# Performance work log

Hardware: AMD Instinct MI355X
Metric: run time of the kernel (lower is better)

The kernel has to match this reference:

```python
import jax, jax.numpy as jnp
import numpy as np

N, N_FEAT, F1, F2, F3, N_Z = 4096, 512, 256, 128, 64, 16
SLOPE = 0.2
NEG = -9e16


def _xavier(key, shape):
    std = (2.0 / (shape[0] + shape[1])) ** 0.5
    return jax.random.normal(key, shape, dtype=jnp.float32) * std


def setup_inputs() -> dict:
    key = jax.random.key(0)
    ks = jax.random.split(key, 20)
    x = jax.random.normal(ks[0], (N, N_FEAT), dtype=jnp.float32)
    adj = jax.random.randint(ks[1], (N, N), 0, 2, dtype=jnp.int32)
    dims = [N_FEAT, F1, F2, F3, N_Z, F3, F2, F1, N_FEAT]
    inp = {"x": x, "adj": adj}
    for i in range(8):
        fi, fo = dims[i], dims[i + 1]
        inp[f"w{i+1}"] = _xavier(ks[2 + 2 * i], (fi, fo))
        inp[f"a{i+1}"] = _xavier(ks[3 + 2 * i], (2 * fo, 1))
    return inp


def _gat(x, adj_pos, w, a):
    h = x @ w                               # [N, f_out]
    f = h.shape[1]
    src = h @ a[:f]                         # [N, 1]
    tgt = h @ a[f:]                         # [N, 1]
    e = jax.nn.leaky_relu(src + tgt.T, SLOPE)  # [N, N] broadcast score sum
    e = jnp.where(adj_pos, e, NEG)
    attn = jax.nn.softmax(e, axis=-1)
    return attn @ h                          # [N, f_out]


def reference(x, adj, w1, a1, w2, a2, w3, a3, w4, a4, w5, a5, w6, a6, w7, a7, w8, a8):
    adj_pos = adj > 0
    h1 = _gat(x, adj_pos, w1, a1)
    h2 = _gat(h1, adj_pos, w2, a2)
    h3 = _gat(h2, adj_pos, w3, a3)
    h4 = _gat(h3, adj_pos, w4, a4)
    h5 = _gat(h4, adj_pos, w5, a5)
    h6 = _gat(h5, adj_pos, w6, a6)
    h7 = _gat(h6, adj_pos, w7, a7)
    x_bar = _gat(h7, adj_pos, w8, a8)
    return (x_bar, h1, h2, h3, h4)
```

## Files before the change

### kernel.cpp

```cpp
#include <hip/hip_runtime.h>
#include <hip/hip_bf16.h>
#include <hip/hip_fp16.h>


#define NROWS 4096
#define TMC 12.0f

typedef __attribute__((ext_vector_type(8))) short v8s;
typedef __attribute__((ext_vector_type(8))) _Float16 v8h;
typedef __attribute__((ext_vector_type(2))) _Float16 h2v;
typedef __attribute__((ext_vector_type(4))) float v4f;

__device__ inline unsigned short f2bf(float x) {
  union { float f; unsigned u; } v; v.f = x;
  unsigned r = v.u + 0x7fffu + ((v.u >> 16) & 1u);
  return (unsigned short)(r >> 16);
}

__global__ void pack_adj(const int* __restrict__ adj, unsigned long long* __restrict__ bits) {
  int row = blockIdx.x;
  int lane = threadIdx.x & 63, wave = threadIdx.x >> 6;
  for (int w = wave; w < 64; w += 4) {
    unsigned long long m = __ballot(adj[(size_t)row * NROWS + w * 64 + lane] > 0);
    if (lane == 0) bits[row * 64 + w] = m;
  }
}

struct WTArgs { const float* src[8]; unsigned short* dst[8]; int K[8]; int F[8]; };
__global__ void transpose_w(WTArgs A) {
  int z = blockIdx.z;
  const float* in = A.src[z];
  unsigned short* out = A.dst[z];
  int R = A.K[z], C = A.F[z];
  __shared__ unsigned short tile[32][33];
  int c0 = blockIdx.x * 32, r0 = blockIdx.y * 32;
  if (c0 >= C || r0 >= R) return;
#pragma unroll
  for (int dy = 0; dy < 32; dy += 8) {
    int r = r0 + threadIdx.y + dy, c = c0 + threadIdx.x;
    if (r < R && c < C) tile[threadIdx.y + dy][threadIdx.x] = f2bf(in[(size_t)r * C + c]);
  }
  __syncthreads();
#pragma unroll
  for (int dy = 0; dy < 32; dy += 8) {
    int c = c0 + threadIdx.y + dy, r = r0 + threadIdx.x;
    if (r < R && c < C) out[(size_t)c * R + r] = tile[threadIdx.x][threadIdx.y + dy];
  }
}

__global__ __launch_bounds__(128) void gemm_xw(const float* __restrict__ A,
                                               const unsigned short* __restrict__ BT,
                                               float* __restrict__ C,
                                               unsigned short* __restrict__ HTt,
                                               int K, int Nf) {
  __shared__ unsigned short zone[64 * 36];
  int lane = threadIdx.x & 63, wave = threadIdx.x >> 6;
  int quad = lane >> 4, l16 = lane & 15;
  int row0 = blockIdx.x * 32 + wave * 16;
  int col0 = blockIdx.y * 64;
  int nf = Nf - col0; nf = nf > 64 ? 4 : (nf + 15) / 16;
  v4f acc[4] = {{0.f,0.f,0.f,0.f},{0.f,0.f,0.f,0.f},{0.f,0.f,0.f,0.f},{0.f,0.f,0.f,0.f}};
  for (int k0 = 0; k0 < K; k0 += 32) {
    int kk = k0 + quad * 8;
    v8s a = {0,0,0,0,0,0,0,0};
    if (kk < K) {
      float4 f0 = *(const float4*)(A + (size_t)(row0 + l16) * K + kk);
      float4 f1 = *(const float4*)(A + (size_t)(row0 + l16) * K + kk + 4);
      union { v8s s; __hip_bfloat162 h[4]; } ua;
      ua.h[0] = __float22bfloat162_rn(make_float2(f0.x, f0.y));
      ua.h[1] = __float22bfloat162_rn(make_float2(f0.z, f0.w));
      ua.h[2] = __float22bfloat162_rn(make_float2(f1.x, f1.y));
      ua.h[3] = __float22bfloat162_rn(make_float2(f1.z, f1.w));
      a = ua.s;
    }
    for (int t = 0; t < nf; t++) {
      v8s b = {0,0,0,0,0,0,0,0};
      if (kk < K) b = *(const v8s*)(BT + (size_t)(col0 + t * 16 + l16) * K + kk);
      acc[t] = __builtin_amdgcn_mfma_f32_16x16x32_bf16(a, b, acc[t], 0, 0, 0);
    }
  }
  for (int t = 0; t < nf; t++) {
#pragma unroll
    for (int r = 0; r < 4; r++) {
      float v = acc[t][r];
      C[(size_t)(row0 + quad * 4 + r) * Nf + col0 + t * 16 + l16] = v;
      union { _Float16 h; unsigned short s; } cv; cv.h = (_Float16)v;
      zone[(t * 16 + l16) * 36 + wave * 16 + quad * 4 + r] = cv.s;
    }
  }
  __syncthreads();
  unsigned* dst = (unsigned*)(HTt + (size_t)(blockIdx.x) * Nf * 32 + (size_t)col0 * 32);
  const unsigned* zsrc = (const unsigned*)zone;
  int total = nf * 256;
  for (int idx = threadIdx.x; idx < total; idx += 128) {
    int f = idx >> 4, jp = idx & 15;
    dst[idx] = zsrc[f * 18 + jp];
  }
}

__global__ void gemv_srctgt(const float* __restrict__ H, const float* __restrict__ a,
                            float* __restrict__ src, unsigned short* __restrict__ Ev16,
                            unsigned short* __restrict__ Gv16, int f) {
  int row = blockIdx.x * 4 + (threadIdx.x >> 6);
  int lane = threadIdx.x & 63;
  float s = 0.f, t = 0.f;
  for (int k = lane; k < f; k += 64) {
    float h = H[(size_t)row * f + k];
    s += h * a[k];
    t += h * a[f + k];
  }
#pragma unroll
  for (int off = 32; off; off >>= 1) { s += __shfl_down(s, off); t += __shfl_down(t, off); }
  if (lane == 0) {
    src[row] = s;
    union { _Float16 h; unsigned short u; } ce, cg;
    ce.h = (_Float16)(__expf(t - TMC) * 16384.f);
    cg.h = (_Float16)(__expf(0.2f * (t - TMC)) * 16.f);
    Ev16[row] = ce.u;
    Gv16[row] = cg.u;
  }
}

template<int NF>
__global__ __launch_bounds__(256) void pass2f(const unsigned* __restrict__ adjW,
                                              const float* __restrict__ src,
                                              const unsigned short* __restrict__ Ev16,
                                              const unsigned short* __restrict__ Gv16,
                                              const unsigned short* __restrict__ HTt,
                                              float* __restrict__ out,
                                              float* __restrict__ part,
                                              float* __restrict__ ls0,
                                              float* __restrict__ part_ls, int F, int js) {
  const int W = NF * 16, Wp = W + 4;
  __shared__ float zone[32 * Wp];
  int lane = threadIdx.x & 63, wave = threadIdx.x >> 6;
  int quad = lane >> 4, l16 = lane & 15;
  int i0 = blockIdx.x * 32;
  int fc0 = blockIdx.y * W;
  const size_t F32 = (size_t)F * 32;
  int jrange = NROWS / js;
  int jlen = jrange / 4;
  int jstart = blockIdx.z * jrange + wave * jlen;

  h2v Ai2[2], Bi2[2];
  const unsigned* arow[2];
#pragma unroll
  for (int ni = 0; ni < 2; ni++) {
    int i = i0 + ni * 16 + l16;
    float sp = src[i] + TMC;
    float m = sp > 0.f ? sp : 0.2f * sp;
    _Float16 ai = (_Float16)(__expf(sp - m) * 0x1p-14f);
    _Float16 bi = (_Float16)(__expf(0.2f * sp - m) * 0x1p-4f);
    Ai2[ni] = (h2v){ai, ai};
    Bi2[ni] = (h2v){bi, bi};
    arow[ni] = adjW + (size_t)i * 128;
  }
  const v8h ones = {(_Float16)1.f, (_Float16)1.f, (_Float16)1.f, (_Float16)1.f,
                    (_Float16)1.f, (_Float16)1.f, (_Float16)1.f, (_Float16)1.f};
  v4f acc[2][NF], accl[2];
#pragma unroll
  for (int ni = 0; ni < 2; ni++) {
    accl[ni] = (v4f){0.f, 0.f, 0.f, 0.f};
#pragma unroll
    for (int t = 0; t < NF; t++) acc[ni][t] = (v4f){0.f, 0.f, 0.f, 0.f};
  }

  for (int j0 = jstart; j0 < jstart + jlen; j0 += 128) {
    uint4 aw[2];
    aw[0] = *(const uint4*)(arow[0] + (j0 >> 5));
    aw[1] = *(const uint4*)(arow[1] + (j0 >> 5));
    unsigned awa[2][4] = {{aw[0].x, aw[0].y, aw[0].z, aw[0].w},
                          {aw[1].x, aw[1].y, aw[1].z, aw[1].w}};
#pragma unroll
    for (int u = 0; u < 4; u++) {
      int ju = j0 + u * 32;
      int jb = ju + quad * 8;
      union { v8s s; h2v h2[4]; } ue, ug;
      ue.s = *(const v8s*)(Ev16 + jb);
      ug.s = *(const v8s*)(Gv16 + jb);
      const unsigned short* bp =
          HTt + (size_t)(ju >> 5) * F32 + (size_t)(fc0 + l16) * 32 + quad * 8;
      union { v8s s; v8h h; } bfr[NF];
#pragma unroll
      for (int t = 0; t < NF; t++) bfr[t].s = *(const v8s*)(bp + t * 512);
#pragma unroll
      for (int ni = 0; ni < 2; ni++) {
        unsigned bb = awa[ni][u] >> (quad * 8);
        union { v8h h; unsigned u32[4]; } ua;
#pragma unroll
        for (int p = 0; p < 4; p++) {
          h2v w2 = __builtin_elementwise_max(Ai2[ni] * ue.h2[p], Bi2[ni] * ug.h2[p]);
          unsigned msk = (((bb >> (2 * p)) & 1u) ? 0x0000FFFFu : 0u)
                       | (((bb >> (2 * p + 1)) & 1u) ? 0xFFFF0000u : 0u);
          union { h2v h2; unsigned u; } tw; tw.h2 = w2;
          ua.u32[p] = tw.u & msk;
        }
#pragma unroll
        for (int t = 0; t < NF; t++)
          acc[ni][t] = __builtin_amdgcn_mfma_f32_16x16x32_f16(ua.h, bfr[t].h, acc[ni][t], 0, 0, 0);
        accl[ni] = __builtin_amdgcn_mfma_f32_16x16x32_f16(ua.h, ones, accl[ni], 0, 0, 0);
      }
    }
  }

  for (int w = 0; w < 4; w++) {
    if (wave == w) {
#pragma unroll
      for (int ni = 0; ni < 2; ni++) {
#pragma unroll
        for (int t = 0; t < NF; t++)
#pragma unroll
          for (int r = 0; r < 4; r++) {
            int idx = (ni * 16 + quad * 4 + r) * Wp + t * 16 + l16;
            if (w == 0) zone[idx] = acc[ni][t][r];
            else        zone[idx] += acc[ni][t][r];
          }
        if (l16 == 0) {
#pragma unroll
          for (int r = 0; r < 4; r++) {
            int idx = (ni * 16 + quad * 4 + r) * Wp + W;
            if (w == 0) zone[idx] = accl[ni][r];
            else        zone[idx] += accl[ni][r];
          }
        }
      }
    }
    __syncthreads();
  }

  if (js == 1) {
    if (threadIdx.x < 32) zone[threadIdx.x * Wp + W] = 1.0f / zone[threadIdx.x * Wp + W];
    __syncthreads();
    for (int idx = threadIdx.x; idx < 32 * W; idx += 256) {
      int rrow = idx / W, ccol = idx - rrow * W;
      out[(size_t)(i0 + rrow) * F + fc0 + ccol] = zone[rrow * Wp + ccol] * zone[rrow * Wp + W];
    }
  } else {
    float* dst = (blockIdx.z == 0) ? out : part + (size_t)(blockIdx.z - 1) * NROWS * F;
    for (int idx = threadIdx.x; idx < 32 * W; idx += 256) {
      int rrow = idx / W, ccol = idx - rrow * W;
      dst[(size_t)(i0 + rrow) * F + fc0 + ccol] = zone[rrow * Wp + ccol];
    }
    if (threadIdx.x < 32) {
      float l = zone[threadIdx.x * Wp + W];
      if (blockIdx.z == 0) ls0[i0 + threadIdx.x] = l;
      else part_ls[(size_t)(blockIdx.z - 1) * NROWS + i0 + threadIdx.x] = l;
    }
  }
}

__global__ void reduce_add(const float* __restrict__ part, const float* __restrict__ part_ls,
                           const float* __restrict__ ls0, float* __restrict__ out, int n, int F,
                           int nslab) {
  int i = blockIdx.x * 256 + threadIdx.x;
  if (i < n) {
    int row = i / F;
    float s = out[i];
    float l = ls0[row];
    for (int z = 0; z < nslab; z++) s += part[(size_t)z * n + i];
    for (int z = 0; z < nslab; z++) l += part_ls[(size_t)z * NROWS + row];
    out[i] = s / l;
  }
}

static void launch_pass2(int NF, dim3 grid, const unsigned* adjW, const float* src,
                         const unsigned short* Ev16, const unsigned short* Gv16,
                         const unsigned short* HTt, float* out, float* part, float* ls0,
                         float* part_ls, int F, int js, hipStream_t stream) {
  switch (NF) {
    case 8: pass2f<8><<<grid, 256, 0, stream>>>(adjW, src, Ev16, Gv16, HTt, out, part, ls0,
                                                part_ls, F, js); break;
    case 4: pass2f<4><<<grid, 256, 0, stream>>>(adjW, src, Ev16, Gv16, HTt, out, part, ls0,
                                                part_ls, F, js); break;
    default: pass2f<1><<<grid, 256, 0, stream>>>(adjW, src, Ev16, Gv16, HTt, out, part, ls0,
                                                 part_ls, F, js); break;
  }
}

extern "C" void kernel_launch(void* const* d_in, const int* in_sizes, int n_in,
                              void* d_out, int out_size, void* d_ws, size_t ws_size,
                              hipStream_t stream) {
  static const int fin[8]  = {512, 256, 128, 64, 16, 64, 128, 256};
  static const int fout[8] = {256, 128, 64, 16, 64, 128, 256, 512};

  const float* x = (const float*)d_in[0];
  const int* adj = (const int*)d_in[1];
  char* ws = (char*)d_ws;
  unsigned long long* bits = (unsigned long long*)(ws);
  unsigned short* WTall = (unsigned short*)(ws + (2u << 20));
  float* H            = (float*)(ws + (6u << 20));
  unsigned short* HTt = (unsigned short*)(ws + (14u << 20));
  float* srcv    = (float*)(ws + (19u << 20));
  float* ls0     = (float*)(ws + (19u << 20) + 49152);
  float* part_ls = (float*)(ws + (19u << 20) + 65536);
  unsigned short* Ev16 = (unsigned short*)(ws + (19u << 20) + 114688);
  unsigned short* Gv16 = (unsigned short*)(ws + (19u << 20) + 122880);
  float* o5    = (float*)(ws + (20u << 20));
  float* o6    = (float*)(ws + (21u << 20));
  float* o7    = (float*)(ws + (23u << 20));
  float* part = H;

  float* outp = (float*)d_out;
  float* xbar = outp;
  float* h1 = outp + (size_t)NROWS * 512;
  float* h2 = h1 + (size_t)NROWS * 256;
  float* h3 = h2 + (size_t)NROWS * 128;
  float* h4 = h3 + (size_t)NROWS * 64;

  float* louts[8] = {h1, h2, h3, h4, o5, o6, o7, xbar};
  const float* lins[8] = {x, h1, h2, h3, h4, o5, o6, o7};

  unsigned short* WT[8];
  { size_t off = 0;
    for (int t = 0; t < 8; t++) { WT[t] = WTall + off; off += (size_t)fin[t] * fout[t]; } }

  pack_adj<<<dim3(4096), dim3(256), 0, stream>>>(adj, bits);

  WTArgs wa;
  for (int t = 0; t < 8; t++) {
    wa.src[t] = (const float*)d_in[2 + 2 * t];
    wa.dst[t] = WT[t];
    wa.K[t] = fin[t];
    wa.F[t] = fout[t];
  }
  transpose_w<<<dim3(16, 16, 8), dim3(32, 8), 0, stream>>>(wa);

  for (int t = 0; t < 8; t++) {
    int K = fin[t], F = fout[t];
    const float* At = (const float*)d_in[3 + 2 * t];
    const float* Xin = lins[t];
    float* Ot = louts[t];

    int NF = F >= 128 ? 8 : (F >= 64 ? 4 : 1);
    int fc = F / (16 * NF);
    int js = (F == 512) ? 1 : (F == 256 ? 2 : 4);

    gemm_xw<<<dim3(128, (F + 63) / 64), dim3(128), 0, stream>>>(Xin, WT[t], H, HTt, K, F);
    gemv_srctgt<<<dim3(1024), dim3(256), 0, stream>>>(H, At, srcv, Ev16, Gv16, F);
    launch_pass2(NF, dim3(128, fc, js), (const unsigned*)bits, srcv, Ev16, Gv16, HTt, Ot, part,
                 ls0, part_ls, F, js, stream);
    if (js > 1)
      reduce_add<<<dim3((NROWS * F + 255) / 256), dim3(256), 0, stream>>>(part, part_ls, ls0, Ot,
                                                                          NROWS * F, F, js - 1);
  }
}
```

Before: 461.4 us.

## Add shared-memory staged attention-aggregation kernel with multi-row-tile reuse for wide layers

Adds pass2s, which stages 64-column tiles of the transposed fp16 H into double-buffered shared memory, prefetching the next tile and the score vectors into registers while the current tile feeds the MFMAs. Each wave handles NI 16-row tiles, so every loaded B fragment is reused across several row tiles. It is used for F of 512, 256 and 128, with the grid and j-split changed (F=512 now splits into two slabs and needs a reduce pass). The aim is fewer global reads of H per output row, at the cost of more registers, block-level syncs and, for F=512, an extra reduction kernel.

```diff
diff --git a/kernel.cpp b/kernel.cpp
--- a/kernel.cpp
+++ b/kernel.cpp
@@ -121,6 +121,159 @@
   }
 }
 
+template<int NF, int NI>
+__global__ __launch_bounds__(256) void pass2s(const unsigned* __restrict__ adjW,
+                                              const float* __restrict__ src,
+                                              const unsigned short* __restrict__ Ev16,
+                                              const unsigned short* __restrict__ Gv16,
+                                              const unsigned short* __restrict__ HTt,
+                                              float* __restrict__ out,
+                                              float* __restrict__ part,
+                                              float* __restrict__ ls0,
+                                              float* __restrict__ part_ls, int F, int js) {
+  constexpr int W = NF * 16;
+  constexpr int LROW = 72;
+  constexpr int SH = (W == 128) ? 9 : (W == 64) ? 8 : 7;
+  constexpr int NCH = (W * 8) / 256;
+  __shared__ unsigned short bs[2][W * LROW];
+
+  int lane = threadIdx.x & 63, wave = threadIdx.x >> 6;
+  int quad = lane >> 4, l16 = lane & 15;
+  int i0 = blockIdx.x * (64 * NI) + wave * (16 * NI);
+  int fc0 = blockIdx.y * W;
+  const size_t F32 = (size_t)F * 32;
+  int jrange = NROWS / js;
+  int nsteps = jrange / 64;
+  int jstart = blockIdx.z * jrange;
+
+  h2v Ai2[NI], Bi2[NI];
+  const unsigned* arow[NI];
+#pragma unroll
+  for (int ni = 0; ni < NI; ni++) {
+    int i = i0 + ni * 16 + l16;
+    float sp = src[i] + TMC;
+    float m = sp > 0.f ? sp : 0.2f * sp;
+    _Float16 ai = (_Float16)(__expf(sp - m) * 0x1p-14f);
+    _Float16 bi = (_Float16)(__expf(0.2f * sp - m) * 0x1p-4f);
+    Ai2[ni] = (h2v){ai, ai};
+    Bi2[ni] = (h2v){bi, bi};
+    arow[ni] = adjW + (size_t)i * 128;
+  }
+  const v8h ones = {(_Float16)1.f, (_Float16)1.f, (_Float16)1.f, (_Float16)1.f,
+                    (_Float16)1.f, (_Float16)1.f, (_Float16)1.f, (_Float16)1.f};
+  v4f acc[NI][NF], accl[NI];
+#pragma unroll
+  for (int ni = 0; ni < NI; ni++) {
+    accl[ni] = (v4f){0.f, 0.f, 0.f, 0.f};
+#pragma unroll
+    for (int t = 0; t < NF; t++) acc[ni][t] = (v4f){0.f, 0.f, 0.f, 0.f};
+  }
+
+  int srcRel[NCH], dstOff[NCH];
+#pragma unroll
+  for (int k = 0; k < NCH; k++) {
+    int g = threadIdx.x + 256 * k;
+    int jt_h = g >> SH;
+    int rem = g & ((W * 4) - 1);
+    int f = rem >> 2, c = rem & 3;
+    srcRel[k] = jt_h * (int)F32 + f * 32 + c * 8;
+    dstOff[k] = f * LROW + jt_h * 32 + c * 8;
+  }
+  const unsigned short* sbase = HTt + ((size_t)(jstart >> 5)) * F32 + (size_t)fc0 * 32;
+
+  v8s sreg[NCH];
+  v8s uePf[2], ugPf[2];
+  uint2 awPf[NI];
+
+#pragma unroll
+  for (int k = 0; k < NCH; k++) sreg[k] = *(const v8s*)(sbase + srcRel[k]);
+#pragma unroll
+  for (int h = 0; h < 2; h++) {
+    uePf[h] = *(const v8s*)(Ev16 + jstart + h * 32 + quad * 8);
+    ugPf[h] = *(const v8s*)(Gv16 + jstart + h * 32 + quad * 8);
+  }
+#pragma unroll
+  for (int ni = 0; ni < NI; ni++) awPf[ni] = *(const uint2*)(arow[ni] + (jstart >> 5));
+#pragma unroll
+  for (int k = 0; k < NCH; k++) *(v8s*)(&bs[0][dstOff[k]]) = sreg[k];
+  __syncthreads();
+
+  int cur = 0;
+  for (int s = 0; s < nsteps; s++) {
+    int j0 = jstart + s * 64;
+    v8s ueL0 = uePf[0], ueL1 = uePf[1], ugL0 = ugPf[0], ugL1 = ugPf[1];
+    uint2 awL[NI];
+#pragma unroll
+    for (int ni = 0; ni < NI; ni++) awL[ni] = awPf[ni];
+
+    if (s + 1 < nsteps) {
+      const unsigned short* sb1 = sbase + (size_t)(s + 1) * 2 * F32;
+#pragma unroll
+      for (int k = 0; k < NCH; k++) sreg[k] = *(const v8s*)(sb1 + srcRel[k]);
+      int j1 = j0 + 64;
+#pragma unroll
+      for (int h = 0; h < 2; h++) {
+        uePf[h] = *(const v8s*)(Ev16 + j1 + h * 32 + quad * 8);
+        ugPf[h] = *(const v8s*)(Gv16 + j1 + h * 32 + quad * 8);
+      }
+#pragma unroll
+      for (int ni = 0; ni < NI; ni++) awPf[ni] = *(const uint2*)(arow[ni] + (j1 >> 5));
+    }
+
+#pragma unroll
+    for (int half = 0; half < 2; half++) {
+      union { v8s s; h2v h2[4]; } ue, ug;
+      ue.s = half ? ueL1 : ueL0;
+      ug.s = half ? ugL1 : ugL0;
+      const unsigned short* lb = &bs[cur][half * 32 + quad * 8];
+      union { v8s s; v8h h; } bfr[NF];
+#pragma unroll
+      for (int t = 0; t < NF; t++) bfr[t].s = *(const v8s*)(lb + (l16 + t * 16) * LROW);
+#pragma unroll
+      for (int ni = 0; ni < NI; ni++) {
+        unsigned bb = (half ? awL[ni].y : awL[ni].x) >> (quad * 8);
+        union { v8h h; unsigned u32[4]; } ua;
+#pragma unroll
+        for (int p = 0; p < 4; p++) {
+          h2v w2 = __builtin_elementwise_max(Ai2[ni] * ue.h2[p], Bi2[ni] * ug.h2[p]);
+          unsigned msk = (((bb >> (2 * p)) & 1u) ? 0x0000FFFFu : 0u)
+                       | (((bb >> (2 * p + 1)) & 1u) ? 0xFFFF0000u : 0u);
+          union { h2v h2; unsigned u; } tw; tw.h2 = w2;
+          ua.u32[p] = tw.u & msk;
+        }
+#pragma unroll
+        for (int t = 0; t < NF; t++)
+          acc[ni][t] = __builtin_amdgcn_mfma_f32_16x16x32_f16(ua.h, bfr[t].h, acc[ni][t], 0, 0, 0);
+        accl[ni] = __builtin_amdgcn_mfma_f32_16x16x32_f16(ua.h, ones, accl[ni], 0, 0, 0);
+      }
+    }
+
+    if (s + 1 < nsteps) {
+#pragma unroll
+      for (int k = 0; k < NCH; k++) *(v8s*)(&bs[cur ^ 1][dstOff[k]]) = sreg[k];
+    }
+    __syncthreads();
+    cur ^= 1;
+  }
+
+  float* dst = (blockIdx.z == 0) ? out : part + (size_t)(blockIdx.z - 1) * NROWS * F;
+#pragma unroll
+  for (int ni = 0; ni < NI; ni++)
+#pragma unroll
+    for (int t = 0; t < NF; t++)
+#pragma unroll
+      for (int r = 0; r < 4; r++)
+        dst[(size_t)(i0 + ni * 16 + quad * 4 + r) * F + fc0 + t * 16 + l16] = acc[ni][t][r];
+  if (l16 == 0) {
+    float* ldst = (blockIdx.z == 0) ? ls0 : part_ls + (size_t)(blockIdx.z - 1) * NROWS;
+#pragma unroll
+    for (int ni = 0; ni < NI; ni++)
+#pragma unroll
+      for (int r = 0; r < 4; r++)
+        ldst[i0 + ni * 16 + quad * 4 + r] = accl[ni][r];
+  }
+}
+
 template<int NF>
 __global__ __launch_bounds__(256) void pass2f(const unsigned* __restrict__ adjW,
                                               const float* __restrict__ src,
@@ -263,20 +416,6 @@
   }
 }
 
-static void launch_pass2(int NF, dim3 grid, const unsigned* adjW, const float* src,
-                         const unsigned short* Ev16, const unsigned short* Gv16,
-                         const unsigned short* HTt, float* out, float* part, float* ls0,
-                         float* part_ls, int F, int js, hipStream_t stream) {
-  switch (NF) {
-    case 8: pass2f<8><<<grid, 256, 0, stream>>>(adjW, src, Ev16, Gv16, HTt, out, part, ls0,
-                                                part_ls, F, js); break;
-    case 4: pass2f<4><<<grid, 256, 0, stream>>>(adjW, src, Ev16, Gv16, HTt, out, part, ls0,
-                                                part_ls, F, js); break;
-    default: pass2f<1><<<grid, 256, 0, stream>>>(adjW, src, Ev16, Gv16, HTt, out, part, ls0,
-                                                 part_ls, F, js); break;
-  }
-}
-
 extern "C" void kernel_launch(void* const* d_in, const int* in_sizes, int n_in,
                               void* d_out, int out_size, void* d_ws, size_t ws_size,
                               hipStream_t stream) {
@@ -331,14 +470,32 @@
     const float* Xin = lins[t];
     float* Ot = louts[t];
 
-    int NF = F >= 128 ? 8 : (F >= 64 ? 4 : 1);
-    int fc = F / (16 * NF);
-    int js = (F == 512) ? 1 : (F == 256 ? 2 : 4);
-
     gemm_xw<<<dim3(128, (F + 63) / 64), dim3(128), 0, stream>>>(Xin, WT[t], H, HTt, K, F);
     gemv_srctgt<<<dim3(1024), dim3(256), 0, stream>>>(H, At, srcv, Ev16, Gv16, F);
-    launch_pass2(NF, dim3(128, fc, js), (const unsigned*)bits, srcv, Ev16, Gv16, HTt, Ot, part,
-                 ls0, part_ls, F, js, stream);
+
+    const unsigned* adjW = (const unsigned*)bits;
+    int js;
+    if (F == 512) {
+      js = 2;
+      pass2s<8, 2><<<dim3(32, 4, js), 256, 0, stream>>>(adjW, srcv, Ev16, Gv16, HTt, Ot, part,
+                                                        ls0, part_ls, F, js);
+    } else if (F == 256) {
+      js = 2;
+      pass2s<8, 1><<<dim3(64, 2, js), 256, 0, stream>>>(adjW, srcv, Ev16, Gv16, HTt, Ot, part,
+                                                        ls0, part_ls, F, js);
+    } else if (F == 128) {
+      js = 4;
+      pass2s<8, 1><<<dim3(64, 1, js), 256, 0, stream>>>(adjW, srcv, Ev16, Gv16, HTt, Ot, part,
+                                                        ls0, part_ls, F, js);
+    } else if (F == 64) {
+      js = 4;
+      pass2f<4><<<dim3(128, 1, js), 256, 0, stream>>>(adjW, srcv, Ev16, Gv16, HTt, Ot, part,
+                                                      ls0, part_ls, F, js);
+    } else {
+      js = 4;
+      pass2f<1><<<dim3(128, 1, js), 256, 0, stream>>>(adjW, srcv, Ev16, Gv16, HTt, Ot, part,
+                                                      ls0, part_ls, F, js);
+    }
     if (js > 1)
       reduce_add<<<dim3((NROWS * F + 255) / 256), dim3(256), 0, stream>>>(part, part_ls, ls0, Ot,
                                                                           NROWS * F, F, js - 1);
```

New measurement: 472.6 us. 2.4% more time.
